# Performance work log

Measured on AMD Instinct MI355X. Metric: run time of the kernel, lower is better.

The kernel has to match this reference:

```python
import jax, jax.numpy as jnp
import numpy as np

V, B, T, C, L, H = 50257, 4, 1024, 768, 12, 12
HS = C // H
EPS = 1e-5


def _ln(x, w, b):
    mu = jnp.mean(x, axis=-1, keepdims=True)
    var = jnp.mean(jnp.square(x - mu), axis=-1, keepdims=True)
    return (x - mu) * jax.lax.rsqrt(var + EPS) * w + b


def setup_inputs() -> dict:
    key = jax.random.key(0)
    ks = jax.random.split(key, 12)
    std = 0.02
    proj_std = 0.02 * (2 * L) ** -0.5  # NANOGPT_SCALE_INIT
    inp = {
        'idx': jax.random.randint(ks[0], (B, T), 0, V),
        'targets': jax.random.randint(ks[1], (B, T), 0, V),
        'wte': jax.random.normal(ks[2], (V, C), jnp.float32) * std,
        'wpe': jax.random.normal(ks[3], (1024, C), jnp.float32) * std,
        'ln1_w': jnp.ones((L, C), jnp.float32),
        'ln1_b': jnp.zeros((L, C), jnp.float32),
        'qkv_w': jax.random.normal(ks[4], (L, C, 3 * C), jnp.float32) * std,
        'qkv_b': jnp.zeros((L, 3 * C), jnp.float32),
        'attn_proj_w': jax.random.normal(ks[5], (L, C, C), jnp.float32) * proj_std,
        'attn_proj_b': jnp.zeros((L, C), jnp.float32),
        'ln2_w': jnp.ones((L, C), jnp.float32),
        'ln2_b': jnp.zeros((L, C), jnp.float32),
        'fc_w': jax.random.normal(ks[6], (L, C, 4 * C), jnp.float32) * std,
        'fc_b': jnp.zeros((L, 4 * C), jnp.float32),
        'mlp_proj_w': jax.random.normal(ks[7], (L, 4 * C, C), jnp.float32) * proj_std,
        'mlp_proj_b': jnp.zeros((L, C), jnp.float32),
        'lnf_w': jnp.ones((C,), jnp.float32),
        'lnf_b': jnp.zeros((C,), jnp.float32),
    }
    return inp


def _gpt(idx, targets, wte, wpe, ln1_w, ln1_b, qkv_w, qkv_b, attn_proj_w,
         attn_proj_b, ln2_w, ln2_b, fc_w, fc_b, mlp_proj_w, mlp_proj_b,
         lnf_w, lnf_b):
    Bx, Tx = idx.shape
    x = wte[idx] + wpe[:Tx]  # [B,T,C]
    mask = jnp.tril(jnp.ones((Tx, Tx), bool))  # causal
    scale = 1.0 / np.sqrt(HS)

    def block(x, p):
        l1w, l1b, qw, qb, pw, pb, l2w, l2b, fw, fb, mw, mb = p
        h = _ln(x, l1w, l1b)
        qkv = h @ qw + qb
        q, k, v = jnp.split(qkv, 3, axis=-1)
        q = q.reshape(Bx, Tx, H, HS)
        k = k.reshape(Bx, Tx, H, HS)
        v = v.reshape(Bx, Tx, H, HS)
        att = jnp.einsum('bqhd,bkhd->bhqk', q, k) * scale
        att = jnp.where(mask, att, -jnp.inf)
        att = jax.nn.softmax(att, axis=-1)
        y = jnp.einsum('bhqk,bkhd->bqhd', att, v).reshape(Bx, Tx, C)
        x = x + y @ pw + pb
        h2 = _ln(x, l2w, l2b)
        x = x + jax.nn.gelu(h2 @ fw + fb, approximate=True) @ mw + mb
        return x, None

    x, _ = jax.lax.scan(block, x, (ln1_w, ln1_b, qkv_w, qkv_b, attn_proj_w,
                                   attn_proj_b, ln2_w, ln2_b, fc_w, fc_b,
                                   mlp_proj_w, mlp_proj_b))
    x = _ln(x, lnf_w, lnf_b)
    logits = x @ wte.T  # tied lm_head, [B,T,V]
    logp = jax.nn.log_softmax(logits, axis=-1)
    nll = -jnp.take_along_axis(logp, targets[..., None], axis=-1)[..., 0]
    loss = jnp.mean(nll)
    return logits, loss


def reference(idx, targets, wte, wpe, ln1_w, ln1_b, qkv_w, qkv_b, attn_proj_w,
              attn_proj_b, ln2_w, ln2_b, fc_w, fc_b, mlp_proj_w, mlp_proj_b,
              lnf_w, lnf_b):
    return _gpt(idx, targets, wte, wpe, ln1_w, ln1_b, qkv_w, qkv_b,
                attn_proj_w, attn_proj_b, ln2_w, ln2_b, fc_w, fc_b,
                mlp_proj_w, mlp_proj_b, lnf_w, lnf_b)
```

## Files before the change

### kernel.cpp

```cpp
#include <hip/hip_runtime.h>
#include <hip/hip_bf16.h>

typedef __attribute__((ext_vector_type(8))) short short8;
typedef __attribute__((ext_vector_type(4))) float f32x4;

static constexpr int VOC = 50257;
static constexpr size_t QKV_T_OFF = 0;
static constexpr size_t AP_T_OFF  = 1769472;
static constexpr size_t FC_T_OFF  = 2359296;
static constexpr size_t MP_T_OFF  = 4718592;
static constexpr size_t LSTR      = 7077888;

__device__ inline unsigned short f2bf(float f){
  unsigned u = __float_as_uint(f);
  unsigned r = (u + 0x7fffu + ((u >> 16) & 1u)) >> 16;
  return (unsigned short)r;
}

__global__ __launch_bounds__(192) void embed_kernel(const int* __restrict__ idx,
    const float* __restrict__ wte, const float* __restrict__ wpe, float* __restrict__ x){
  int row = blockIdx.x;
  int t = row & 1023;
  int id = idx[row];
  const float* w = wte + (size_t)id * 768;
  const float* p = wpe + (size_t)t * 768;
  float* o = x + (size_t)row * 768;
  int c = threadIdx.x * 4;
  float4 a = *(const float4*)(w + c);
  float4 b = *(const float4*)(p + c);
  float4 r; r.x = a.x + b.x; r.y = a.y + b.y; r.z = a.z + b.z; r.w = a.w + b.w;
  *(float4*)(o + c) = r;
}

__global__ __launch_bounds__(256) void ln_kernel(const float* __restrict__ x,
    const float* __restrict__ w, const float* __restrict__ b,
    unsigned short* __restrict__ out){
  __shared__ float red[4];
  int row = blockIdx.x, tid = threadIdx.x;
  const float* xr = x + (size_t)row * 768;
  float v0 = xr[tid], v1 = xr[tid + 256], v2 = xr[tid + 512];
  float s = v0 + v1 + v2;
  #pragma unroll
  for (int o = 32; o; o >>= 1) s += __shfl_xor(s, o, 64);
  if ((tid & 63) == 0) red[tid >> 6] = s;
  __syncthreads();
  s = red[0] + red[1] + red[2] + red[3];
  float mu = s * (1.f / 768.f);
  float d0 = v0 - mu, d1 = v1 - mu, d2 = v2 - mu;
  float q = d0 * d0 + d1 * d1 + d2 * d2;
  __syncthreads();
  #pragma unroll
  for (int o = 32; o; o >>= 1) q += __shfl_xor(q, o, 64);
  if ((tid & 63) == 0) red[tid >> 6] = q;
  __syncthreads();
  q = red[0] + red[1] + red[2] + red[3];
  float rstd = rsqrtf(q * (1.f / 768.f) + 1e-5f);
  unsigned short* orow = out + (size_t)row * 768;
  orow[tid]       = f2bf(d0 * rstd * w[tid]       + b[tid]);
  orow[tid + 256] = f2bf(d1 * rstd * w[tid + 256] + b[tid + 256]);
  orow[tid + 512] = f2bf(d2 * rstd * w[tid + 512] + b[tid + 512]);
}

__global__ void transpose_all(const float* __restrict__ qkvw, const float* __restrict__ apw,
    const float* __restrict__ fcw, const float* __restrict__ mpw,
    unsigned short* __restrict__ dst){
  __shared__ float t[32][33];
  int l = blockIdx.y;
  int tile = blockIdx.x;
  const float* W; unsigned short* D; int K, N, ntx, tl;
  if (tile < 1728){      W = qkvw + (size_t)l * 768 * 2304; D = dst + (size_t)l * LSTR + QKV_T_OFF; K = 768;  N = 2304; ntx = 72; tl = tile; }
  else if (tile < 2304){ W = apw  + (size_t)l * 768 * 768;  D = dst + (size_t)l * LSTR + AP_T_OFF;  K = 768;  N = 768;  ntx = 24; tl = tile - 1728; }
  else if (tile < 4608){ W = fcw  + (size_t)l * 768 * 3072; D = dst + (size_t)l * LSTR + FC_T_OFF;  K = 768;  N = 3072; ntx = 96; tl = tile - 2304; }
  else {                 W = mpw  + (size_t)l * 3072 * 768; D = dst + (size_t)l * LSTR + MP_T_OFF;  K = 3072; N = 768;  ntx = 24; tl = tile - 4608; }
  int n0 = (tl % ntx) * 32, k0 = (tl / ntx) * 32;
  int tx = threadIdx.x, ty = threadIdx.y;
  #pragma unroll
  for (int i = 0; i < 4; i++)
    t[ty + i * 8][tx] = W[(size_t)(k0 + ty + i * 8) * N + n0 + tx];
  __syncthreads();
  #pragma unroll
  for (int i = 0; i < 4; i++)
    D[(size_t)(n0 + ty + i * 8) * K + k0 + tx] = f2bf(t[tx][ty + i * 8]);
}

__global__ void cvt_bf16_kernel(const float* __restrict__ src, unsigned short* __restrict__ dst, int n4){
  int i = blockIdx.x * blockDim.x + threadIdx.x;
  int stride = gridDim.x * blockDim.x;
  for (; i < n4; i += stride){
    float4 v = *(const float4*)(src + (size_t)i * 4);
    size_t o = (size_t)i * 4;
    dst[o + 0] = f2bf(v.x); dst[o + 1] = f2bf(v.y);
    dst[o + 2] = f2bf(v.z); dst[o + 3] = f2bf(v.w);
  }
}

#define GEMM256_MAIN_LOOP(CLAMP_B)                                                  \
  f32x4 acc[4][4];                                                                  \
  _Pragma("unroll")                                                                 \
  for (int m = 0; m < 4; m++)                                                       \
    _Pragma("unroll")                                                               \
    for (int n = 0; n < 4; n++)                                                     \
      acc[m][n] = (f32x4){0.f, 0.f, 0.f, 0.f};                                      \
  for (int k0 = 0; k0 < K; k0 += 64){                                               \
    _Pragma("unroll")                                                               \
    for (int i = 0; i < 4; i++){                                                    \
      int p = (i * 8 + wid) * 64 + lane;                                            \
      int r = p >> 3, c = p & 7;                                                    \
      int cs = c ^ (r & 7);                                                         \
      const unsigned short* g = A + (size_t)(brow + r) * K + k0 + cs * 8;           \
      __builtin_amdgcn_global_load_lds(                                             \
        (const __attribute__((address_space(1))) unsigned int*)g,                   \
        (__attribute__((address_space(3))) unsigned int*)(tA + (size_t)(i * 8 + wid) * 64 * 8), \
        16, 0, 0);                                                                  \
    }                                                                               \
    _Pragma("unroll")                                                               \
    for (int i = 0; i < 2; i++){                                                    \
      int p = (i * 8 + wid) * 64 + lane;                                            \
      int r = p >> 3, c = p & 7;                                                    \
      int cs = c ^ (r & 7);                                                         \
      int rc = CLAMP_B;                                                             \
      const unsigned short* g = Bm + (size_t)(bcol + rc) * K + k0 + cs * 8;         \
      __builtin_amdgcn_global_load_lds(                                             \
        (const __attribute__((address_space(1))) unsigned int*)g,                   \
        (__attribute__((address_space(3))) unsigned int*)(tB + (size_t)(i * 8 + wid) * 64 * 8), \
        16, 0, 0);                                                                  \
    }                                                                               \
    __syncthreads();                                                                \
    _Pragma("unroll")                                                               \
    for (int kk = 0; kk < 2; kk++){                                                 \
      short8 av[4], bv[4];                                                          \
      _Pragma("unroll")                                                             \
      for (int m = 0; m < 4; m++){                                                  \
        int R = wr * 64 + m * 16 + lr;                                              \
        int c = kk * 4 + lk;                                                        \
        av[m] = *(const short8*)&tA[R * 64 + ((c ^ (R & 7)) << 3)];                 \
      }                                                                             \
      _Pragma("unroll")                                                             \
      for (int n = 0; n < 4; n++){                                                  \
        int R = wc * 64 + n * 16 + lr;                                              \
        int c = kk * 4 + lk;                                                        \
        bv[n] = *(const short8*)&tB[R * 64 + ((c ^ (R & 7)) << 3)];                 \
      }                                                                             \
      _Pragma("unroll")                                                             \
      for (int m = 0; m < 4; m++)                                                   \
        _Pragma("unroll")                                                           \
        for (int n = 0; n < 4; n++)                                                 \
          acc[m][n] = __builtin_amdgcn_mfma_f32_16x16x32_bf16(av[m], bv[n], acc[m][n], 0, 0, 0); \
    }                                                                               \
    __syncthreads();                                                                \
  }

__global__ __launch_bounds__(512) void gemm_fc256(
    const unsigned short* __restrict__ A,
    const unsigned short* __restrict__ Bm,
    const float* __restrict__ bias,
    unsigned short* __restrict__ outB,
    int M, int N, int K)
{
  __shared__ unsigned short tA[16384];
  __shared__ unsigned short tB[8192];
  const int lane = threadIdx.x & 63;
  const int wid  = threadIdx.x >> 6;
  const int wr = wid >> 1, wc = wid & 1;
  const int lr = lane & 15, lk = lane >> 4;
  const int nbx = gridDim.x, nby = gridDim.y;
  const int nwg = nbx * nby;
  const int lin = blockIdx.y * nbx + blockIdx.x;
  const int qq = nwg >> 3, rr8 = nwg & 7;
  const int xcd = lin & 7, loc = lin >> 3;
  const int wg = (xcd < rr8 ? xcd * (qq + 1) : rr8 * (qq + 1) + (xcd - rr8) * qq) + loc;
  const int mblk = wg / nbx, nblk = wg % nbx;
  const int brow = mblk * 256;
  const int bcol = nblk * 128;

  GEMM256_MAIN_LOOP(r)

  #pragma unroll
  for (int m = 0; m < 4; m++){
    #pragma unroll
    for (int n = 0; n < 4; n++){
      int col = bcol + wc * 64 + n * 16 + lr;
      float bco = bias[col];
      #pragma unroll
      for (int j = 0; j < 4; j++){
        int row = brow + wr * 64 + m * 16 + lk * 4 + j;
        float v = acc[m][n][j] + bco;
        float x3 = v * v * v;
        v = 0.5f * v * (1.f + tanhf(0.79788456080286536f * (v + 0.044715f * x3)));
        outB[(size_t)row * N + col] = f2bf(v);
      }
    }
  }
}

__global__ __launch_bounds__(512) void gemm_qkv256(
    const unsigned short* __restrict__ A,
    const unsigned short* __restrict__ Bm,
    const float* __restrict__ bias,
    unsigned short* __restrict__ Qb,
    unsigned short* __restrict__ Kb,
    unsigned short* __restrict__ VT,
    int M, int N, int K)
{
  __shared__ unsigned short tA[16384];
  __shared__ unsigned short tB[8192];
  const int lane = threadIdx.x & 63;
  const int wid  = threadIdx.x >> 6;
  const int wr = wid >> 1, wc = wid & 1;
  const int lr = lane & 15, lk = lane >> 4;
  const int nbx = gridDim.x, nby = gridDim.y;
  const int nwg = nbx * nby;
  const int lin = blockIdx.y * nbx + blockIdx.x;
  const int qq = nwg >> 3, rr8 = nwg & 7;
  const int xcd = lin & 7, loc = lin >> 3;
  const int wg = (xcd < rr8 ? xcd * (qq + 1) : rr8 * (qq + 1) + (xcd - rr8) * qq) + loc;
  const int mblk = wg / nbx, nblk = wg % nbx;
  const int brow = mblk * 256;
  const int bcol = nblk * 128;

  GEMM256_MAIN_LOOP(r)

  const int b = brow >> 10, tstart = brow & 1023;
  if (bcol < 1536){
    #pragma unroll
    for (int m = 0; m < 4; m++)
      #pragma unroll
      for (int n = 0; n < 4; n++){
        int col = bcol + wc * 64 + n * 16 + lr;
        float bco = bias[col];
        int isK = col >= 768;
        int h = (isK ? col - 768 : col) >> 6;
        unsigned short* dstp = isK ? Kb : Qb;
        #pragma unroll
        for (int j = 0; j < 4; j++){
          int t = tstart + wr * 64 + m * 16 + lk * 4 + j;
          dstp[(((size_t)b * 12 + h) * 1024 + t) * 64 + (col & 63)] =
              f2bf(acc[m][n][j] + bco);
        }
      }
  } else {
    unsigned short* sh = tA;
    const int h0 = (bcol - 1536) >> 6;
    #pragma unroll
    for (int half = 0; half < 4; half++){
      __syncthreads();
      if (wr == half){
        #pragma unroll
        for (int m = 0; m < 4; m++)
          #pragma unroll
          for (int n = 0; n < 4; n++){
            int lcol = wc * 64 + n * 16 + lr;
            float bco = bias[bcol + lcol];
            #pragma unroll
            for (int j = 0; j < 4; j++)
              sh[(m * 16 + lk * 4 + j) * 136 + lcol] = f2bf(acc[m][n][j] + bco);
          }
      }
      __syncthreads();
      int c_local = threadIdx.x & 127, tpart = threadIdx.x >> 7;
      int h = h0 + (c_local >> 6);
      int d = c_local & 63;
      unsigned short* vrow = VT + (((size_t)b * 12 + h) * 64 + d) * 1024
                           + tstart + half * 64 + tpart * 16;
      #pragma unroll
      for (int i = 0; i < 2; i++){
        short8 pk;
        #pragma unroll
        for (int s2 = 0; s2 < 8; s2++)
          pk[s2] = (short)sh[(tpart * 16 + i * 8 + s2) * 136 + c_local];
        *(short8*)&vrow[i * 8] = pk;
      }
    }
  }
}

__global__ __launch_bounds__(256) void gemm_n64(
    const unsigned short* __restrict__ A,
    const unsigned short* __restrict__ Bm,
    const float* __restrict__ bias,
    const float* __restrict__ resid,
    float* __restrict__ outF,
    int M, int N, int K)
{
  __shared__ unsigned short tA[8192];
  __shared__ unsigned short tB[4096];
  const int lane = threadIdx.x & 63;
  const int wid  = threadIdx.x >> 6;
  const int wr = wid >> 1, wc = wid & 1;
  const int lr = lane & 15, lk = lane >> 4;
  const int nbx = gridDim.x, nby = gridDim.y;
  const int nwg = nbx * nby;
  const int lin = blockIdx.y * nbx + blockIdx.x;
  const int qq = nwg >> 3, rr8 = nwg & 7;
  const int xcd = lin & 7, loc = lin >> 3;
  const int wg = (xcd < rr8 ? xcd * (qq + 1) : rr8 * (qq + 1) + (xcd - rr8) * qq) + loc;
  const int mblk = wg / nbx, nblk = wg % nbx;
  const int brow = mblk * 128;
  const int bcol = nblk * 64;

  f32x4 acc[4][2];
  #pragma unroll
  for (int m = 0; m < 4; m++)
    #pragma unroll
    for (int n = 0; n < 2; n++)
      acc[m][n] = (f32x4){0.f, 0.f, 0.f, 0.f};

  for (int k0 = 0; k0 < K; k0 += 64){
    #pragma unroll
    for (int i = 0; i < 4; i++){
      int p = (i * 4 + wid) * 64 + lane;
      int r = p >> 3, c = p & 7;
      int cs = c ^ (r & 7);
      const unsigned short* g = A + (size_t)(brow + r) * K + k0 + cs * 8;
      __builtin_amdgcn_global_load_lds(
        (const __attribute__((address_space(1))) unsigned int*)g,
        (__attribute__((address_space(3))) unsigned int*)(tA + (size_t)(i * 4 + wid) * 64 * 8),
        16, 0, 0);
    }
    #pragma unroll
    for (int i = 0; i < 2; i++){
      int p = (i * 4 + wid) * 64 + lane;
      int r = p >> 3, c = p & 7;
      int cs = c ^ (r & 7);
      const unsigned short* g = Bm + (size_t)(bcol + r) * K + k0 + cs * 8;
      __builtin_amdgcn_global_load_lds(
        (const __attribute__((address_space(1))) unsigned int*)g,
        (__attribute__((address_space(3))) unsigned int*)(tB + (size_t)(i * 4 + wid) * 64 * 8),
        16, 0, 0);
    }
    __syncthreads();
    #pragma unroll
    for (int kk = 0; kk < 2; kk++){
      short8 av[4], bv[2];
      #pragma unroll
      for (int m = 0; m < 4; m++){
        int R = wr * 64 + m * 16 + lr;
        int c = kk * 4 + lk;
        av[m] = *(const short8*)&tA[R * 64 + ((c ^ (R & 7)) << 3)];
      }
      #pragma unroll
      for (int n = 0; n < 2; n++){
        int R = wc * 32 + n * 16 + lr;
        int c = kk * 4 + lk;
        bv[n] = *(const short8*)&tB[R * 64 + ((c ^ (R & 7)) << 3)];
      }
      #pragma unroll
      for (int m = 0; m < 4; m++)
        #pragma unroll
        for (int n = 0; n < 2; n++)
          acc[m][n] = __builtin_amdgcn_mfma_f32_16x16x32_bf16(av[m], bv[n], acc[m][n], 0, 0, 0);
    }
    __syncthreads();
  }

  #pragma unroll
  for (int m = 0; m < 4; m++){
    #pragma unroll
    for (int n = 0; n < 2; n++){
      int col = bcol + wc * 32 + n * 16 + lr;
      float bco = bias[col];
      #pragma unroll
      for (int j = 0; j < 4; j++){
        int row = brow + wr * 64 + m * 16 + lk * 4 + j;
        float v = acc[m][n][j] + bco + resid[(size_t)row * N + col];
        outF[(size_t)row * N + col] = v;
      }
    }
  }
}

__global__ __launch_bounds__(512) void gemm_head(
    const unsigned short* __restrict__ A,
    const unsigned short* __restrict__ Bm,
    float* __restrict__ outF,
    float2* __restrict__ lossPart,
    int M, int N, int K, int nPart)
{
  __shared__ unsigned short tA[16384];
  __shared__ unsigned short tB[8192];
  const int lane = threadIdx.x & 63;
  const int wid  = threadIdx.x >> 6;
  const int wr = wid >> 1, wc = wid & 1;
  const int lr = lane & 15, lk = lane >> 4;
  const int nblk = blockIdx.x, mblk = blockIdx.y;
  const int brow = mblk * 256;
  const int bcol = nblk * 128;
  const int nValid = N - bcol;

  GEMM256_MAIN_LOOP(r < nValid ? r : (nValid - 1))

  #pragma unroll
  for (int m = 0; m < 4; m++){
    #pragma unroll
    for (int n = 0; n < 4; n++){
      int col = bcol + wc * 64 + n * 16 + lr;
      if (col < N){
        #pragma unroll
        for (int j = 0; j < 4; j++){
          int row = brow + wr * 64 + m * 16 + lk * 4 + j;
          outF[(size_t)row * N + col] = acc[m][n][j];
        }
      }
    }
  }

  float* mred = (float*)tA;
  float* sred = mred + 512;
  #pragma unroll
  for (int m = 0; m < 4; m++){
    #pragma unroll
    for (int j = 0; j < 4; j++){
      float vv[4];
      float mx = -3.4e38f;
      #pragma unroll
      for (int n = 0; n < 4; n++){
        int col = bcol + wc * 64 + n * 16 + lr;
        vv[n] = (col < N) ? acc[m][n][j] : -3.4e38f;
        mx = fmaxf(mx, vv[n]);
      }
      #pragma unroll
      for (int msk = 1; msk < 16; msk <<= 1)
        mx = fmaxf(mx, __shfl_xor(mx, msk, 64));
      float sm = 0.f;
      #pragma unroll
      for (int n = 0; n < 4; n++){
        int col = bcol + wc * 64 + n * 16 + lr;
        if (col < N) sm += __expf(vv[n] - mx);
      }
      #pragma unroll
      for (int msk = 1; msk < 16; msk <<= 1)
        sm += __shfl_xor(sm, msk, 64);
      if (lr == 0){
        int rid = (wr * 2 + wc) * 64 + m * 16 + lk * 4 + j;
        mred[rid] = mx; sred[rid] = sm;
      }
    }
  }
  __syncthreads();
  if (threadIdx.x < 256){
    int wrq = threadIdx.x >> 6, rowi = threadIdx.x & 63;
    float m0 = mred[(wrq * 2 + 0) * 64 + rowi];
    float m1 = mred[(wrq * 2 + 1) * 64 + rowi];
    float s0 = sred[(wrq * 2 + 0) * 64 + rowi];
    float s1 = sred[(wrq * 2 + 1) * 64 + rowi];
    float Mv = fmaxf(m0, m1);
    float Sv = (s0 > 0.f ? s0 * __expf(m0 - Mv) : 0.f)
             + (s1 > 0.f ? s1 * __expf(m1 - Mv) : 0.f);
    int grow = brow + wrq * 64 + rowi;
    lossPart[(size_t)grow * nPart + nblk] = make_float2(Mv, Sv);
  }
}

__global__ __launch_bounds__(256) void attn_mfma(
    const unsigned short* __restrict__ Qb,
    const unsigned short* __restrict__ Kb,
    const unsigned short* __restrict__ VT,
    unsigned short* __restrict__ y)
{
  __shared__ unsigned short Kl[64 * 64];
  __shared__ unsigned short Vl[64 * 64];
  __shared__ unsigned short Pl[4][16 * 72];
  const int xq = blockIdx.x;
  const int qt = (xq & 1) ? (xq >> 1) : (15 - (xq >> 1));
  const int h = blockIdx.y, b = blockIdx.z;
  const size_t bh = (size_t)(b * 12 + h);
  const int lane = threadIdx.x & 63;
  const int w = threadIdx.x >> 6;
  const int lr = lane & 15, lk = lane >> 4;

  short8 aq[2];
  {
    const unsigned short* qrow = Qb + ((bh * 1024) + qt * 64 + w * 16 + lr) * 64;
    aq[0] = *(const short8*)&qrow[lk * 8];
    aq[1] = *(const short8*)&qrow[32 + lk * 8];
  }

  f32x4 o[4];
  #pragma unroll
  for (int n = 0; n < 4; n++) o[n] = (f32x4){0.f, 0.f, 0.f, 0.f};
  float mold[4] = {-1e30f, -1e30f, -1e30f, -1e30f};
  float lsum[4] = {0.f, 0.f, 0.f, 0.f};

  for (int kt = 0; kt <= qt; kt++){
    #pragma unroll
    for (int i = 0; i < 2; i++){
      int p = (i * 4 + w) * 64 + lane;
      int r = p >> 3, c = p & 7;
      int cs = c ^ (r & 7);
      const unsigned short* gk = Kb + (bh * 1024 + (size_t)kt * 64 + r) * 64 + cs * 8;
      __builtin_amdgcn_global_load_lds(
        (const __attribute__((address_space(1))) unsigned int*)gk,
        (__attribute__((address_space(3))) unsigned int*)(Kl + (size_t)(i * 4 + w) * 64 * 8),
        16, 0, 0);
      const unsigned short* gv = VT + (bh * 64 + r) * 1024 + (size_t)kt * 64 + cs * 8;
      __builtin_amdgcn_global_load_lds(
        (const __attribute__((address_space(1))) unsigned int*)gv,
        (__attribute__((address_space(3))) unsigned int*)(Vl + (size_t)(i * 4 + w) * 64 * 8),
        16, 0, 0);
    }
    __syncthreads();

    f32x4 s[4];
    #pragma unroll
    for (int n = 0; n < 4; n++) s[n] = (f32x4){0.f, 0.f, 0.f, 0.f};
    #pragma unroll
    for (int ck = 0; ck < 2; ck++){
      #pragma unroll
      for (int n = 0; n < 4; n++){
        int R = n * 16 + lr, c = ck * 4 + lk;
        short8 bv = *(const short8*)&Kl[R * 64 + ((c ^ (R & 7)) << 3)];
        s[n] = __builtin_amdgcn_mfma_f32_16x16x32_bf16(aq[ck], bv, s[n], 0, 0, 0);
      }
    }
    #pragma unroll
    for (int n = 0; n < 4; n++)
      #pragma unroll
      for (int j = 0; j < 4; j++){
        float v = s[n][j] * 0.125f;
        if (kt == qt && (n * 16 + lr) > (w * 16 + lk * 4 + j)) v = -1e30f;
        s[n][j] = v;
      }
    float mt[4];
    #pragma unroll
    for (int j = 0; j < 4; j++)
      mt[j] = fmaxf(fmaxf(s[0][j], s[1][j]), fmaxf(s[2][j], s[3][j]));
    #pragma unroll
    for (int msk = 1; msk < 16; msk <<= 1)
      #pragma unroll
      for (int j = 0; j < 4; j++)
        mt[j] = fmaxf(mt[j], __shfl_xor(mt[j], msk, 64));
    #pragma unroll
    for (int j = 0; j < 4; j++){
      float mn = fmaxf(mold[j], mt[j]);
      float a = __expf(mold[j] - mn);
      mold[j] = mn;
      lsum[j] *= a;
      #pragma unroll
      for (int n = 0; n < 4; n++){
        float p = __expf(s[n][j] - mn);
        s[n][j] = p;
        lsum[j] += p;
      }
      #pragma unroll
      for (int n2 = 0; n2 < 4; n2++) o[n2][j] *= a;
    }
    #pragma unroll
    for (int n = 0; n < 4; n++)
      #pragma unroll
      for (int j = 0; j < 4; j++)
        Pl[w][(lk * 4 + j) * 72 + n * 16 + lr] = f2bf(s[n][j]);
    __syncthreads();
    #pragma unroll
    for (int ck = 0; ck < 2; ck++){
      short8 pa = *(const short8*)&Pl[w][lr * 72 + ck * 32 + lk * 8];
      #pragma unroll
      for (int n2 = 0; n2 < 4; n2++){
        int R = n2 * 16 + lr, c = ck * 4 + lk;
        short8 vv = *(const short8*)&Vl[R * 64 + ((c ^ (R & 7)) << 3)];
        o[n2] = __builtin_amdgcn_mfma_f32_16x16x32_bf16(pa, vv, o[n2], 0, 0, 0);
      }
    }
    __syncthreads();
  }

  #pragma unroll
  for (int msk = 1; msk < 16; msk <<= 1)
    #pragma unroll
    for (int j = 0; j < 4; j++)
      lsum[j] += __shfl_xor(lsum[j], msk, 64);
  float inv[4];
  #pragma unroll
  for (int j = 0; j < 4; j++) inv[j] = 1.f / lsum[j];

  #pragma unroll
  for (int n2 = 0; n2 < 4; n2++)
    #pragma unroll
    for (int j = 0; j < 4; j++){
      size_t row = (size_t)(b * 1024 + qt * 64 + w * 16 + lk * 4 + j);
      y[row * 768 + h * 64 + n2 * 16 + lr] = f2bf(o[n2][j] * inv[j]);
    }
}

__global__ __launch_bounds__(64) void loss_rows2(const float2* __restrict__ part,
    const float* __restrict__ logits, const int* __restrict__ targets,
    float* __restrict__ nll, int nPart){
  int row = blockIdx.x, lane = threadIdx.x;
  float m = -3.4e38f, s = 0.f;
  for (int i = lane; i < nPart; i += 64){
    float2 p = part[(size_t)row * nPart + i];
    if (p.y > 0.f){
      float nm = fmaxf(m, p.x);
      s = s * __expf(m - nm) + p.y * __expf(p.x - nm);
      m = nm;
    }
  }
  #pragma unroll
  for (int o = 32; o; o >>= 1){
    float m2 = __shfl_xor(m, o, 64);
    float s2 = __shfl_xor(s, o, 64);
    float nm = fmaxf(m, m2);
    s = s * __expf(m - nm) + s2 * __expf(m2 - nm);
    m = nm;
  }
  if (lane == 0)
    nll[row] = m + logf(s) - logits[(size_t)row * VOC + targets[row]];
}

__global__ __launch_bounds__(256) void loss_final(const float* __restrict__ nll,
                                                  float* __restrict__ out){
  __shared__ float red[4];
  int tid = threadIdx.x;
  float s = 0.f;
  for (int i = tid; i < 4096; i += 256) s += nll[i];
  #pragma unroll
  for (int o = 32; o; o >>= 1) s += __shfl_xor(s, o, 64);
  if ((tid & 63) == 0) red[tid >> 6] = s;
  __syncthreads();
  if (tid == 0) out[0] = (red[0] + red[1] + red[2] + red[3]) * (1.f / 4096.f);
}

extern "C" void kernel_launch(void* const* d_in, const int* in_sizes, int n_in,
                              void* d_out, int out_size, void* d_ws, size_t ws_size,
                              hipStream_t stream){
  (void)in_sizes; (void)n_in; (void)out_size;
  const int*   idx     = (const int*)d_in[0];
  const int*   targets = (const int*)d_in[1];
  const float* wte     = (const float*)d_in[2];
  const float* wpe     = (const float*)d_in[3];
  const float* ln1w    = (const float*)d_in[4];
  const float* ln1b    = (const float*)d_in[5];
  const float* qkvw    = (const float*)d_in[6];
  const float* qkvb    = (const float*)d_in[7];
  const float* apw     = (const float*)d_in[8];
  const float* apb     = (const float*)d_in[9];
  const float* ln2w    = (const float*)d_in[10];
  const float* ln2b    = (const float*)d_in[11];
  const float* fcw     = (const float*)d_in[12];
  const float* fcb     = (const float*)d_in[13];
  const float* mpw     = (const float*)d_in[14];
  const float* mpb     = (const float*)d_in[15];
  const float* lnfw    = (const float*)d_in[16];
  const float* lnfb    = (const float*)d_in[17];

  char* ws = (char*)d_ws;
  size_t off = 0;
  auto alloc = [&](size_t bytes){
    void* p = ws + off; off += (bytes + 255) & ~(size_t)255; return p;
  };
  float* x               = (float*)alloc((size_t)4096 * 768 * 4);
  unsigned short* hbf    = (unsigned short*)alloc((size_t)4096 * 768 * 2);
  unsigned short* ybf    = (unsigned short*)alloc((size_t)4096 * 768 * 2);
  unsigned short* gbf    = (unsigned short*)alloc((size_t)4096 * 3072 * 2);
  unsigned short* wtebf  = (unsigned short*)alloc((size_t)VOC * 768 * 2);
  unsigned short* qb     = (unsigned short*)alloc((size_t)48 * 1024 * 64 * 2);
  unsigned short* kbf    = (unsigned short*)alloc((size_t)48 * 1024 * 64 * 2);
  unsigned short* vtb    = (unsigned short*)alloc((size_t)48 * 1024 * 64 * 2);
  float2* lossPart       = (float2*)alloc((size_t)4096 * 393 * 8);
  float* nll             = (float*)alloc((size_t)4096 * 4);
  bool mega = (ws_size - off) >= (12 * LSTR * 2 + 256);
  unsigned short* wTall = (unsigned short*)alloc(mega ? 12 * LSTR * 2 : LSTR * 2);

  float* logits  = (float*)d_out;
  float* lossOut = logits + (size_t)4096 * VOC;

  cvt_bf16_kernel<<<2048, 256, 0, stream>>>(wte, wtebf, (VOC * 768) / 4);
  embed_kernel<<<4096, 192, 0, stream>>>(idx, wte, wpe, x);
  if (mega)
    transpose_all<<<dim3(6912, 12), dim3(32, 8), 0, stream>>>(qkvw, apw, fcw, mpw, wTall);

  for (int l = 0; l < 12; l++){
    unsigned short* wTl = wTall;
    if (mega) wTl = wTall + (size_t)l * LSTR;
    else
      transpose_all<<<dim3(6912, 1), dim3(32, 8), 0, stream>>>(
          qkvw + (size_t)l * 768 * 2304, apw + (size_t)l * 768 * 768,
          fcw + (size_t)l * 768 * 3072, mpw + (size_t)l * 3072 * 768, wTall);

    ln_kernel<<<4096, 256, 0, stream>>>(x, ln1w + l * 768, ln1b + l * 768, hbf);
    gemm_qkv256<<<dim3(2304 / 128, 4096 / 256), 512, 0, stream>>>(
        hbf, wTl + QKV_T_OFF, qkvb + l * 2304, qb, kbf, vtb, 4096, 2304, 768);
    attn_mfma<<<dim3(16, 12, 4), 256, 0, stream>>>(qb, kbf, vtb, ybf);
    gemm_n64<<<dim3(768 / 64, 4096 / 128), 256, 0, stream>>>(
        ybf, wTl + AP_T_OFF, apb + l * 768, x, x, 4096, 768, 768);
    ln_kernel<<<4096, 256, 0, stream>>>(x, ln2w + l * 768, ln2b + l * 768, hbf);
    gemm_fc256<<<dim3(3072 / 128, 4096 / 256), 512, 0, stream>>>(
        hbf, wTl + FC_T_OFF, fcb + l * 3072, gbf, 4096, 3072, 768);
    gemm_n64<<<dim3(768 / 64, 4096 / 128), 256, 0, stream>>>(
        gbf, wTl + MP_T_OFF, mpb + l * 768, x, x, 4096, 768, 3072);
  }
  ln_kernel<<<4096, 256, 0, stream>>>(x, lnfw, lnfb, hbf);
  gemm_head<<<dim3((VOC + 127) / 128, 4096 / 256), 512, 0, stream>>>(
      hbf, wtebf, logits, lossPart, 4096, VOC, 768, (VOC + 127) / 128);
  loss_rows2<<<4096, 64, 0, stream>>>(lossPart, logits, targets, nll, (VOC + 127) / 128);
  loss_final<<<1, 256, 0, stream>>>(nll, lossOut);
}
```

Before: 3.034 ms.

## Use wave-per-row LayerNorm, fast GELU tanh, and smaller-tile attention projection GEMM

LayerNorm now assigns one wavefront per row with float4 loads, shuffle-only reductions and vectorized bf16 stores, removing shared memory and block barriers. The GELU epilogue in the FC GEMM replaces tanhf with an exp-based tanh formula. The attention output projection uses a new 64x64-tile GEMM that launches more workgroups, giving the 768-wide output better occupancy. The exp-based tanh changes rounding slightly, and the smaller tile reuses fewer operands per load.

```diff
diff --git a/kernel.cpp b/kernel.cpp
--- a/kernel.cpp
+++ b/kernel.cpp
@@ -2,6 +2,7 @@
 #include <hip/hip_bf16.h>
 
 typedef __attribute__((ext_vector_type(8))) short short8;
+typedef __attribute__((ext_vector_type(4))) short shortv4;
 typedef __attribute__((ext_vector_type(4))) float f32x4;
 
 static constexpr int VOC = 50257;
@@ -35,30 +36,37 @@
 __global__ __launch_bounds__(256) void ln_kernel(const float* __restrict__ x,
     const float* __restrict__ w, const float* __restrict__ b,
     unsigned short* __restrict__ out){
-  __shared__ float red[4];
-  int row = blockIdx.x, tid = threadIdx.x;
+  int row  = blockIdx.x * 4 + (threadIdx.x >> 6);
+  int lane = threadIdx.x & 63;
   const float* xr = x + (size_t)row * 768;
-  float v0 = xr[tid], v1 = xr[tid + 256], v2 = xr[tid + 512];
-  float s = v0 + v1 + v2;
+  float4 v0 = *(const float4*)(xr + lane * 4);
+  float4 v1 = *(const float4*)(xr + 256 + lane * 4);
+  float4 v2 = *(const float4*)(xr + 512 + lane * 4);
+  float s = (v0.x + v0.y + v0.z + v0.w) + (v1.x + v1.y + v1.z + v1.w)
+          + (v2.x + v2.y + v2.z + v2.w);
   #pragma unroll
   for (int o = 32; o; o >>= 1) s += __shfl_xor(s, o, 64);
-  if ((tid & 63) == 0) red[tid >> 6] = s;
-  __syncthreads();
-  s = red[0] + red[1] + red[2] + red[3];
   float mu = s * (1.f / 768.f);
-  float d0 = v0 - mu, d1 = v1 - mu, d2 = v2 - mu;
-  float q = d0 * d0 + d1 * d1 + d2 * d2;
-  __syncthreads();
+  float q =
+    (v0.x-mu)*(v0.x-mu) + (v0.y-mu)*(v0.y-mu) + (v0.z-mu)*(v0.z-mu) + (v0.w-mu)*(v0.w-mu) +
+    (v1.x-mu)*(v1.x-mu) + (v1.y-mu)*(v1.y-mu) + (v1.z-mu)*(v1.z-mu) + (v1.w-mu)*(v1.w-mu) +
+    (v2.x-mu)*(v2.x-mu) + (v2.y-mu)*(v2.y-mu) + (v2.z-mu)*(v2.z-mu) + (v2.w-mu)*(v2.w-mu);
   #pragma unroll
   for (int o = 32; o; o >>= 1) q += __shfl_xor(q, o, 64);
-  if ((tid & 63) == 0) red[tid >> 6] = q;
-  __syncthreads();
-  q = red[0] + red[1] + red[2] + red[3];
   float rstd = rsqrtf(q * (1.f / 768.f) + 1e-5f);
   unsigned short* orow = out + (size_t)row * 768;
-  orow[tid]       = f2bf(d0 * rstd * w[tid]       + b[tid]);
-  orow[tid + 256] = f2bf(d1 * rstd * w[tid + 256] + b[tid + 256]);
-  orow[tid + 512] = f2bf(d2 * rstd * w[tid + 512] + b[tid + 512]);
+  #pragma unroll
+  for (int seg = 0; seg < 3; seg++){
+    float4 v = seg == 0 ? v0 : (seg == 1 ? v1 : v2);
+    float4 wv = *(const float4*)(w + seg * 256 + lane * 4);
+    float4 bv = *(const float4*)(b + seg * 256 + lane * 4);
+    shortv4 o4;
+    o4[0] = (short)f2bf((v.x - mu) * rstd * wv.x + bv.x);
+    o4[1] = (short)f2bf((v.y - mu) * rstd * wv.y + bv.y);
+    o4[2] = (short)f2bf((v.z - mu) * rstd * wv.z + bv.z);
+    o4[3] = (short)f2bf((v.w - mu) * rstd * wv.w + bv.w);
+    *(shortv4*)(orow + seg * 256 + lane * 4) = o4;
+  }
 }
 
 __global__ void transpose_all(const float* __restrict__ qkvw, const float* __restrict__ apw,
@@ -185,8 +193,12 @@
       for (int j = 0; j < 4; j++){
         int row = brow + wr * 64 + m * 16 + lk * 4 + j;
         float v = acc[m][n][j] + bco;
-        float x3 = v * v * v;
-        v = 0.5f * v * (1.f + tanhf(0.79788456080286536f * (v + 0.044715f * x3)));
+        float z = 0.79788456080286536f * (v + 0.044715f * v * v * v);
+        float az = fabsf(z);
+        float e = __expf(-2.f * az);
+        float t = (1.f - e) / (1.f + e);
+        t = z < 0.f ? -t : t;
+        v = 0.5f * v * (1.f + t);
         outB[(size_t)row * N + col] = f2bf(v);
       }
     }
@@ -369,6 +381,95 @@
   }
 }
 
+__global__ __launch_bounds__(256) void gemm_n64s(
+    const unsigned short* __restrict__ A,
+    const unsigned short* __restrict__ Bm,
+    const float* __restrict__ bias,
+    const float* __restrict__ resid,
+    float* __restrict__ outF,
+    int M, int N, int K)
+{
+  __shared__ unsigned short tA[4096];
+  __shared__ unsigned short tB[4096];
+  const int lane = threadIdx.x & 63;
+  const int wid  = threadIdx.x >> 6;
+  const int wr = wid >> 1, wc = wid & 1;
+  const int lr = lane & 15, lk = lane >> 4;
+  const int nbx = gridDim.x, nby = gridDim.y;
+  const int nwg = nbx * nby;
+  const int lin = blockIdx.y * nbx + blockIdx.x;
+  const int qq = nwg >> 3, rr8 = nwg & 7;
+  const int xcd = lin & 7, loc = lin >> 3;
+  const int wg = (xcd < rr8 ? xcd * (qq + 1) : rr8 * (qq + 1) + (xcd - rr8) * qq) + loc;
+  const int mblk = wg / nbx, nblk = wg % nbx;
+  const int brow = mblk * 64;
+  const int bcol = nblk * 64;
+
+  f32x4 acc[2][2];
+  #pragma unroll
+  for (int m = 0; m < 2; m++)
+    #pragma unroll
+    for (int n = 0; n < 2; n++)
+      acc[m][n] = (f32x4){0.f, 0.f, 0.f, 0.f};
+
+  for (int k0 = 0; k0 < K; k0 += 64){
+    #pragma unroll
+    for (int i = 0; i < 2; i++){
+      int p = (i * 4 + wid) * 64 + lane;
+      int r = p >> 3, c = p & 7;
+      int cs = c ^ (r & 7);
+      const unsigned short* ga = A + (size_t)(brow + r) * K + k0 + cs * 8;
+      __builtin_amdgcn_global_load_lds(
+        (const __attribute__((address_space(1))) unsigned int*)ga,
+        (__attribute__((address_space(3))) unsigned int*)(tA + (size_t)(i * 4 + wid) * 64 * 8),
+        16, 0, 0);
+      const unsigned short* gb = Bm + (size_t)(bcol + r) * K + k0 + cs * 8;
+      __builtin_amdgcn_global_load_lds(
+        (const __attribute__((address_space(1))) unsigned int*)gb,
+        (__attribute__((address_space(3))) unsigned int*)(tB + (size_t)(i * 4 + wid) * 64 * 8),
+        16, 0, 0);
+    }
+    __syncthreads();
+    #pragma unroll
+    for (int kk = 0; kk < 2; kk++){
+      short8 av[2], bv[2];
+      #pragma unroll
+      for (int m = 0; m < 2; m++){
+        int R = wr * 32 + m * 16 + lr;
+        int c = kk * 4 + lk;
+        av[m] = *(const short8*)&tA[R * 64 + ((c ^ (R & 7)) << 3)];
+      }
+      #pragma unroll
+      for (int n = 0; n < 2; n++){
+        int R = wc * 32 + n * 16 + lr;
+        int c = kk * 4 + lk;
+        bv[n] = *(const short8*)&tB[R * 64 + ((c ^ (R & 7)) << 3)];
+      }
+      #pragma unroll
+      for (int m = 0; m < 2; m++)
+        #pragma unroll
+        for (int n = 0; n < 2; n++)
+          acc[m][n] = __builtin_amdgcn_mfma_f32_16x16x32_bf16(av[m], bv[n], acc[m][n], 0, 0, 0);
+    }
+    __syncthreads();
+  }
+
+  #pragma unroll
+  for (int m = 0; m < 2; m++){
+    #pragma unroll
+    for (int n = 0; n < 2; n++){
+      int col = bcol + wc * 32 + n * 16 + lr;
+      float bco = bias[col];
+      #pragma unroll
+      for (int j = 0; j < 4; j++){
+        int row = brow + wr * 32 + m * 16 + lk * 4 + j;
+        float v = acc[m][n][j] + bco + resid[(size_t)row * N + col];
+        outF[(size_t)row * N + col] = v;
+      }
+    }
+  }
+}
+
 __global__ __launch_bounds__(512) void gemm_head(
     const unsigned short* __restrict__ A,
     const unsigned short* __restrict__ Bm,
@@ -676,19 +777,19 @@
           qkvw + (size_t)l * 768 * 2304, apw + (size_t)l * 768 * 768,
           fcw + (size_t)l * 768 * 3072, mpw + (size_t)l * 3072 * 768, wTall);
 
-    ln_kernel<<<4096, 256, 0, stream>>>(x, ln1w + l * 768, ln1b + l * 768, hbf);
+    ln_kernel<<<1024, 256, 0, stream>>>(x, ln1w + l * 768, ln1b + l * 768, hbf);
     gemm_qkv256<<<dim3(2304 / 128, 4096 / 256), 512, 0, stream>>>(
         hbf, wTl + QKV_T_OFF, qkvb + l * 2304, qb, kbf, vtb, 4096, 2304, 768);
     attn_mfma<<<dim3(16, 12, 4), 256, 0, stream>>>(qb, kbf, vtb, ybf);
-    gemm_n64<<<dim3(768 / 64, 4096 / 128), 256, 0, stream>>>(
+    gemm_n64s<<<dim3(768 / 64, 4096 / 64), 256, 0, stream>>>(
         ybf, wTl + AP_T_OFF, apb + l * 768, x, x, 4096, 768, 768);
-    ln_kernel<<<4096, 256, 0, stream>>>(x, ln2w + l * 768, ln2b + l * 768, hbf);
+    ln_kernel<<<1024, 256, 0, stream>>>(x, ln2w + l * 768, ln2b + l * 768, hbf);
     gemm_fc256<<<dim3(3072 / 128, 4096 / 256), 512, 0, stream>>>(
         hbf, wTl + FC_T_OFF, fcb + l * 3072, gbf, 4096, 3072, 768);
     gemm_n64<<<dim3(768 / 64, 4096 / 128), 256, 0, stream>>>(
         gbf, wTl + MP_T_OFF, mpb + l * 768, x, x, 4096, 768, 3072);
   }
-  ln_kernel<<<4096, 256, 0, stream>>>(x, lnfw, lnfb, hbf);
+  ln_kernel<<<1024, 256, 0, stream>>>(x, lnfw, lnfb, hbf);
   gemm_head<<<dim3((VOC + 127) / 128, 4096 / 256), 512, 0, stream>>>(
       hbf, wtebf, logits, lossPart, 4096, VOC, 768, (VOC + 127) / 128);
   loss_rows2<<<4096, 64, 0, stream>>>(lossPart, logits, targets, nll, (VOC + 127) / 128);
```

Result: faster. 2.946 ms (-2.9%).
